# Kernel optimization log

Hardware: AMD Instinct MI355X
Metric: run time of the kernel (lower is better)

The kernel has to match this reference:

```python
import jax, jax.numpy as jnp
import numpy as np

EPS = 1e-3  # Keras BatchNormalization default epsilon


def _conv2d_same(x, w):
    # x: [N,H,W,Cin], w: [kh,kw,Cin,Cout]
    return jax.lax.conv_general_dilated(
        x, w, window_strides=(1, 1), padding='SAME',
        dimension_numbers=('NHWC', 'HWIO', 'NHWC'))


def _hard_sigmoid(x):
    return jnp.clip(0.2 * x + 0.5, 0.0, 1.0)


def _convlstm2d(x, Wx, Wh, b):
    # x: [B,T,H,W,Cin]; Wx: [3,3,Cin,4F]; Wh: [3,3,F,4F]; b: [4F]
    B, T, H, W, Cin = x.shape
    F = Wh.shape[2]
    # precompute input-to-gate convs for all timesteps at once
    xg = _conv2d_same(x.reshape(B * T, H, W, Cin), Wx).reshape(B, T, H, W, 4 * F) + b

    def step(carry, xt):
        h, c = carry
        g = xt + _conv2d_same(h, Wh)
        gi, gf, gc, go = jnp.split(g, 4, axis=-1)  # Keras gate order i,f,c,o
        i = _hard_sigmoid(gi)
        f = _hard_sigmoid(gf)
        o = _hard_sigmoid(go)
        c = f * c + i * jnp.tanh(gc)
        h = o * jnp.tanh(c)
        return (h, c), h

    h0 = jnp.zeros((B, H, W, F), x.dtype)
    (_, _), hs = jax.lax.scan(step, (h0, h0), jnp.moveaxis(xg, 1, 0))
    return jnp.moveaxis(hs, 0, 1)  # [B,T,H,W,F]


def _batchnorm(x, g, be, m, v):
    # inference-mode BN over channel axis
    return (x - m) * (g * jax.lax.rsqrt(v + EPS)) + be


def setup_inputs() -> dict:
    key = jax.random.key(0)
    ks = jax.random.split(key, 10)
    B, T, H, W, C, F, NC = 16, 64, 16, 16, 6, 96, 10
    s = 0.05
    x = jax.random.normal(ks[0], (B, T, H, W, C), jnp.float32)
    Wx0 = jax.random.normal(ks[1], (3, 3, C, 4 * F), jnp.float32) * s
    Wh0 = jax.random.normal(ks[2], (3, 3, F, 4 * F), jnp.float32) * s
    b0 = jnp.zeros((4 * F,), jnp.float32)
    g0 = jnp.ones((F,), jnp.float32)
    be0 = jnp.zeros((F,), jnp.float32)
    m0 = jax.random.normal(ks[3], (F,), jnp.float32) * 0.1
    v0 = jax.random.uniform(ks[4], (F,), jnp.float32) + 0.5
    Wx1 = jax.random.normal(ks[5], (3, 3, F, 4 * F), jnp.float32) * s
    Wh1 = jax.random.normal(ks[6], (3, 3, F, 4 * F), jnp.float32) * s
    b1 = jnp.zeros((4 * F,), jnp.float32)
    g1 = jnp.ones((F,), jnp.float32)
    be1 = jnp.zeros((F,), jnp.float32)
    m1 = jax.random.normal(ks[7], (F,), jnp.float32) * 0.1
    v1 = jax.random.uniform(ks[8], (F,), jnp.float32) + 0.5
    Wd = jax.random.normal(ks[9], (T * H * W * F, NC), jnp.float32) * 0.001
    bd = jnp.zeros((NC,), jnp.float32)
    return dict(x=x, Wx0=Wx0, Wh0=Wh0, b0=b0, g0=g0, be0=be0, m0=m0, v0=v0,
                Wx1=Wx1, Wh1=Wh1, b1=b1, g1=g1, be1=be1, m1=m1, v1=v1,
                Wd=Wd, bd=bd)


def reference(x, Wx0, Wh0, b0, g0, be0, m0, v0,
              Wx1, Wh1, b1, g1, be1, m1, v1, Wd, bd):
    h = _convlstm2d(x, Wx0, Wh0, b0)
    h = _batchnorm(h, g0, be0, m0, v0)
    h = _convlstm2d(h, Wx1, Wh1, b1)
    h = _batchnorm(h, g1, be1, m1, v1)
    B = h.shape[0]
    flat = h.reshape(B, -1)  # Keras Flatten (row-major, channels-last)
    return flat @ Wd + bd
```

## Files before the change

kernel.cpp:

```cpp
#include <hip/hip_runtime.h>
#include <math.h>


typedef __attribute__((ext_vector_type(8))) short     bf16x8;
typedef __attribute__((ext_vector_type(8))) unsigned short u16x8;
typedef __attribute__((ext_vector_type(4))) float     f32x4;
typedef unsigned short u16;

#define RS 393216

__device__ __forceinline__ float hsig(float x) {
    return fminf(fmaxf(0.2f * x + 0.5f, 0.0f), 1.0f);
}
__device__ __forceinline__ float bf2f(u16 u) {
    union { unsigned int i; float f; } v; v.i = ((unsigned int)u) << 16; return v.f;
}
__device__ __forceinline__ u16 f2bf(float f) {
    union { float f; unsigned int i; } v; v.f = f;
    unsigned int r = (v.i + 0x7FFFu + ((v.i >> 16) & 1u)) >> 16;
    return (u16)r;
}

__device__ __forceinline__ void gridbar(unsigned* ctrs, unsigned* epoch,
                                        unsigned k, int blk)
{
    __syncthreads();
    if (threadIdx.x == 0) {
        __builtin_amdgcn_fence(__ATOMIC_RELEASE, "agent");
        __hip_atomic_fetch_add(ctrs + (blk & 63) * 64, 1u,
                               __ATOMIC_RELAXED, __HIP_MEMORY_SCOPE_AGENT);
    }
    if (blk == 0 && threadIdx.x < 64) {
        const unsigned target = k * 256u;
        unsigned sum;
        do {
            unsigned v = __hip_atomic_load(ctrs + threadIdx.x * 64,
                                           __ATOMIC_RELAXED,
                                           __HIP_MEMORY_SCOPE_AGENT);
            sum = v;
#pragma unroll
            for (int m = 1; m < 64; m <<= 1)
                sum += __shfl_xor(sum, m, 64);
            if (sum < target) __builtin_amdgcn_s_sleep(2);
        } while (sum < target);
        if (threadIdx.x == 0)
            __hip_atomic_store(epoch, k, __ATOMIC_RELAXED,
                               __HIP_MEMORY_SCOPE_AGENT);
    }
    if (threadIdx.x == 0) {
        while (__hip_atomic_load(epoch, __ATOMIC_RELAXED,
                                 __HIP_MEMORY_SCOPE_AGENT) < k)
            __builtin_amdgcn_s_sleep(4);
        __builtin_amdgcn_fence(__ATOMIC_ACQUIRE, "agent");
    }
    __syncthreads();
}

__device__ __forceinline__ void xbar(unsigned* slots, int myslot,
                                     unsigned target)
{
    __syncthreads();
    if (threadIdx.x == 0)
        __hip_atomic_fetch_add(slots + myslot * 32, 1u,
                               __ATOMIC_RELAXED, __HIP_MEMORY_SCOPE_AGENT);
    if (threadIdx.x < 32) {
        unsigned sum;
        do {
            unsigned v = __hip_atomic_load(slots + threadIdx.x * 32,
                                           __ATOMIC_RELAXED,
                                           __HIP_MEMORY_SCOPE_AGENT);
            sum = v;
#pragma unroll
            for (int m = 1; m < 32; m <<= 1)
                sum += __shfl_xor(sum, m, 64);
            if (sum < target) __builtin_amdgcn_s_sleep(2);
        } while (sum < target);
        asm volatile("buffer_inv sc0\n\ts_waitcnt vmcnt(0)" ::: "memory");
    }
    __syncthreads();
}

__global__ __launch_bounds__(256) void prep_x(const float* __restrict__ x,
                                              u16* __restrict__ xpad)
{
    const int idx = blockIdx.x * 256 + threadIdx.x;
    const int t = idx >> 12, b = (idx >> 8) & 15, p = idx & 255;
    const float* src = x + (((size_t)b * 64 + t) * 256 + p) * 6;
    u16x8 v = {};
    v[0] = f2bf(src[0]); v[1] = f2bf(src[1]); v[2] = f2bf(src[2]);
    v[3] = f2bf(src[3]); v[4] = f2bf(src[4]); v[5] = f2bf(src[5]);
    *(u16x8*)(xpad + (size_t)idx * 8) = v;
}

__global__ __launch_bounds__(256) void wtransF0(const float* __restrict__ Wx0,
                                                const float* __restrict__ Wh0,
                                                u16* __restrict__ W)
{
    const int idx = blockIdx.x * 256 + threadIdx.x;
    const int e = idx & 7;
    const int lane = (idx >> 3) & 63;
    int r = idx >> 9;
    const int nf = r % 3; r /= 3;
    const int wn = r & 1; r >>= 1;
    const int ks = r % 30;
    const int nt = r / 30;
    const int fr = lane & 15, fg = lane >> 4;
    const int jl = wn * 48 + nf * 16 + fr;
    const int no = (jl / 24) * 96 + nt * 24 + (jl % 24);
    const int k = ks * 32 + fg * 8 + e;
    float v = 0.0f;
    if (k < 96) {
        const int q = k >> 3, c = k & 7;
        if (q < 9 && c < 6) v = Wx0[(q * 6 + c) * 384 + no];
    } else {
        v = Wh0[(k - 96) * 384 + no];
    }
    W[idx] = f2bf(v);
}

__global__ __launch_bounds__(256) void wtransF1(const float* __restrict__ Wx1,
                                                const float* __restrict__ Wh1,
                                                u16* __restrict__ W)
{
    const int idx = blockIdx.x * 256 + threadIdx.x;
    const int e = idx & 7;
    const int lane = (idx >> 3) & 63;
    int r = idx >> 9;
    const int nf = r % 3; r /= 3;
    const int wn = r & 1; r >>= 1;
    const int ks = r % 54;
    const int nt = r / 54;
    const int fr = lane & 15, fg = lane >> 4;
    const int jl = wn * 48 + nf * 16 + fr;
    const int no = (jl / 24) * 96 + nt * 24 + (jl % 24);
    const int k = ks * 32 + fg * 8 + e;
    const float v = (k < 864) ? Wx1[k * 384 + no] : Wh1[(k - 864) * 384 + no];
    W[idx] = f2bf(v);
}

__global__ __launch_bounds__(256) void wtransD(const float* __restrict__ Wd,
                                               u16* __restrict__ WdT)
{
    const int k = blockIdx.x * 256 + threadIdx.x;
    const float* src = Wd + (size_t)k * 10;
#pragma unroll
    for (int nc = 0; nc < 10; ++nc)
        WdT[(size_t)nc * 1572864 + k] = f2bf(src[nc]);
}

__device__ void phase(int t, int m0, int n0, int tidx, char* lds,
    const u16* __restrict__ xpad, u16* __restrict__ h0b,
    u16* __restrict__ h1b, u16* __restrict__ h0bnb, u16* __restrict__ hall,
    const u16* __restrict__ WtF0, const u16* __restrict__ WtF1,
    const float* __restrict__ b0, const float* __restrict__ b1,
    const float* __restrict__ g0, const float* __restrict__ be0,
    const float* __restrict__ mu0, const float* __restrict__ v0,
    const float* __restrict__ g1, const float* __restrict__ be1,
    const float* __restrict__ mu1, const float* __restrict__ v1,
    float (&cregs)[6])
{
    const int half = tidx >> 8;
    const int htid = tidx & 255;
    const bool active = half ? (t < 63) : (t >= 0);

    const u16* in0 = half ? (xpad + (size_t)(t + 1) * 32768)
                          : (h0bnb + (size_t)(t & 1) * RS);
    const u16* in1 = half ? (h0b + (size_t)(t & 1) * RS)
                          : (h1b + (size_t)((t - 1) & 1) * RS);
    u16* hraw_out = half ? (h0b + (size_t)((t + 1) & 1) * RS)
                         : (h1b + (size_t)(t & 1) * RS);
    u16* hbn_out  = half ? (h0bnb + (size_t)((t + 1) & 1) * RS)
                         : (hall + (size_t)(t < 0 ? 0 : t) * RS);

    const int lane = htid & 63;
    const int hw   = htid >> 6;
    const int wm = hw >> 1, wn = hw & 1;
    const int fr = lane & 15, fg = lane >> 4;
    const int arow = htid >> 2, seg = htid & 3;
    const int mg = m0 + arow;
    const int py = (mg >> 4) & 15, px = mg & 15, pb = mg >> 8;
    const int nt = n0 / 96;

    const int   NS0  = half ? 3   : 27;
    const int   MYST = half ? 30  : 54;
    const u16*  Bp   = (half ? WtF0 : WtF1)
                       + (size_t)nt * (MYST * 3072) + wn * 1536 + (lane << 3);

    u16*   AsH  = (u16*)(lds + half * 25600);
    float* accS = (float*)(lds + half * 25600);

    f32x4 acc[2][3];
#pragma unroll
    for (int i = 0; i < 2; ++i)
#pragma unroll
        for (int j = 0; j < 3; ++j) acc[i][j] = (f32x4){0.f, 0.f, 0.f, 0.f};

    auto stageA = [&](int ks, u16x8& va) {
        u16x8 z = {};
        va = z;
        if (half && ks < 3) {
            const int q = ks * 4 + seg;
            const int qd = q / 3;
            const int yy = py + qd - 1;
            const int xx = px + (q - 3 * qd) - 1;
            if (q < 9 && (unsigned)yy < 16u && (unsigned)xx < 16u)
                va = *(const u16x8*)(in0 + (size_t)((pb << 8) + yy * 16 + xx) * 8);
        } else {
            const int s = (ks < NS0) ? ks : ks - NS0;
            const u16* src = (ks < NS0) ? in0 : in1;
            const int q = s / 3;
            const int c0v = (s - 3 * q) * 32 + seg * 8;
            const int qd = q / 3;
            const int yy = py + qd - 1;
            const int xx = px + (q - 3 * qd) - 1;
            if ((unsigned)yy < 16u && (unsigned)xx < 16u)
                va = *(const u16x8*)(src + (size_t)((pb << 8) + yy * 16 + xx) * 96 + c0v);
        }
    };
    auto ldswA = [&](int buf, u16x8& va) {
        *(u16x8*)(AsH + buf * 2560 + arow * 40 + seg * 8) = va;
    };
    auto loadB = [&](int ks, bf16x8 (&bq)[3]) {
#pragma unroll
        for (int nf = 0; nf < 3; ++nf)
            bq[nf] = *(const bf16x8*)(Bp + ks * 3072 + nf * 512);
    };
    auto dofrag = [&](int buf, bf16x8 (&bq)[3]) {
        const u16* A = AsH + buf * 2560;
        bf16x8 af[2];
#pragma unroll
        for (int mf = 0; mf < 2; ++mf)
            af[mf] = *(const bf16x8*)(A + (wm * 32 + mf * 16 + fr) * 40 + fg * 8);

        __builtin_amdgcn_s_setprio(1);
#pragma unroll
        for (int mf = 0; mf < 2; ++mf)
#pragma unroll
            for (int nf = 0; nf < 3; ++nf)
                acc[mf][nf] = __builtin_amdgcn_mfma_f32_16x16x32_bf16(
                    af[mf], bq[nf], acc[mf][nf], 0, 0, 0);
        __builtin_amdgcn_s_setprio(0);
    };

    u16x8 vaA, vaB;
    bf16x8 bqE[3], bqO[3], tE[3], tO[3];

    if (active) {
        stageA(0, vaA); stageA(1, vaB);
        ldswA(0, vaA);  ldswA(1, vaB);
        loadB(0, bqE);  loadB(1, bqO);
    }
    __syncthreads();

    for (int j = 0; j < 27; ++j) {
        const int ks = 2 * j;
        if (active && ks < MYST) {
            const bool more = (ks + 2 < MYST);
            if (more) {
                stageA(ks + 2, vaA);
                stageA(ks + 3, vaB);
                loadB(ks + 2, tE);
                loadB(ks + 3, tO);
            }
            dofrag(ks & 3, bqE);
            dofrag((ks + 1) & 3, bqO);
            if (more) {
                ldswA((ks + 2) & 3, vaA);
                ldswA((ks + 3) & 3, vaB);
#pragma unroll
                for (int nf = 0; nf < 3; ++nf) {
                    bqE[nf] = tE[nf];
                    bqO[nf] = tO[nf];
                }
            }
        }
        __syncthreads();
    }

    if (active) {
        const float* bias = half ? b0 : b1;
#pragma unroll
        for (int nf = 0; nf < 3; ++nf) {
            const int col = wn * 48 + nf * 16 + fr;
            const float bi = bias[(col / 24) * 96 + nt * 24 + (col % 24)];
#pragma unroll
            for (int mf = 0; mf < 2; ++mf) {
                const int row = wm * 32 + mf * 16 + fg * 4;
#pragma unroll
                for (int r = 0; r < 4; ++r)
                    accS[(row + r) * 100 + col] = acc[mf][nf][r] + bi;
            }
        }
    }
    __syncthreads();

    if (active) {
        const float* gam = half ? g0 : g1;
        const float* bet = half ? be0 : be1;
        const float* muv = half ? mu0 : mu1;
        const float* var = half ? v0  : v1;
#pragma unroll
        for (int q = 0; q < 6; ++q) {
            const int item = htid + 256 * q;
            const int r = item / 24, fl = item - r * 24;
            const float gi = accS[r * 100 + fl];
            const float gf = accS[r * 100 + 24 + fl];
            const float gc = accS[r * 100 + 48 + fl];
            const float go = accS[r * 100 + 72 + fl];
            const int f = nt * 24 + fl;
            const float i_ = hsig(gi);
            const float f_ = hsig(gf);
            const float o_ = hsig(go);
            const float c_ = f_ * cregs[q] + i_ * tanhf(gc);
            const float h_ = o_ * tanhf(c_);
            cregs[q] = c_;
            hraw_out[(size_t)(m0 + r) * 96 + f] = f2bf(h_);
            const float s = gam[f] * rsqrtf(var[f] + 1e-3f);
            hbn_out[(size_t)(m0 + r) * 96 + f] =
                f2bf((h_ - muv[f]) * s + bet[f]);
        }
    }
}

__global__ __launch_bounds__(512, 1) void fused(
    unsigned* bctrs, unsigned* bepoch, unsigned* reg8, unsigned* xslots,
    const u16* xpad, u16* h0b, u16* h1b, u16* h0bnb, u16* hall,
    const u16* WtF0, const u16* WtF1,
    const float* b0, const float* b1,
    const float* g0, const float* be0, const float* mu0, const float* v0,
    const float* g1, const float* be1, const float* mu1, const float* v1)
{
    __shared__ char lds[51200];
    __shared__ unsigned shinfo[3];
    const int blk = blockIdx.x;

    if (threadIdx.x == 0) {
        unsigned xcc;
        asm volatile("s_getreg_b32 %0, hwreg(HW_REG_XCC_ID)" : "=s"(xcc));
        xcc &= 7u;
        unsigned slot = __hip_atomic_fetch_add(reg8 + xcc * 64, 1u,
                                               __ATOMIC_RELAXED,
                                               __HIP_MEMORY_SCOPE_AGENT);
        shinfo[0] = xcc; shinfo[1] = slot;
    }
    gridbar(bctrs, bepoch, 1, blk);
    if (threadIdx.x == 0) {
        unsigned ok = 1;
#pragma unroll
        for (int k = 0; k < 8; ++k)
            ok &= (__hip_atomic_load(reg8 + k * 64, __ATOMIC_RELAXED,
                                     __HIP_MEMORY_SCOPE_AGENT) == 32u);
        shinfo[2] = ok;
    }
    __syncthreads();
    const unsigned grp  = shinfo[0];
    const unsigned slot = shinfo[1];
    const bool grouped  = (shinfo[2] != 0u);

    float cregs[6] = {0.f, 0.f, 0.f, 0.f, 0.f, 0.f};

    if (grouped) {
        const int m0 = (int)grp * 512 + (int)(slot >> 2) * 64;
        const int n0 = (int)(slot & 3) * 96;
        unsigned* gs = xslots + grp * 1024;
        unsigned bar = 0;
        for (int t = -1; t < 64; ++t) {
            phase(t, m0, n0, threadIdx.x, lds, xpad, h0b, h1b, h0bnb, hall,
                  WtF0, WtF1, b0, b1, g0, be0, mu0, v0, g1, be1, mu1, v1,
                  cregs);
            xbar(gs, (int)slot, (++bar) * 32u);
        }
    } else {
        const int m0 = (blk >> 2) * 64;
        const int n0 = (blk & 3) * 96;
        unsigned bar = 1;
        for (int t = -1; t < 64; ++t) {
            phase(t, m0, n0, threadIdx.x, lds, xpad, h0b, h1b, h0bnb, hall,
                  WtF0, WtF1, b0, b1, g0, be0, mu0, v0, g1, be1, mu1, v1,
                  cregs);
            gridbar(bctrs, bepoch, ++bar, blk);
        }
    }
}

__global__ __launch_bounds__(512, 1) void stepF(int t,
    const u16* xpad, u16* h0b, u16* h1b, u16* h0bnb, u16* hall,
    const u16* WtF0, const u16* WtF1,
    const float* b0, const float* b1,
    const float* g0, const float* be0, const float* mu0, const float* v0,
    const float* g1, const float* be1, const float* mu1, const float* v1,
    float* c0g, float* c1g)
{
    __shared__ char lds[51200];
    const int m0 = (blockIdx.x >> 2) * 64;
    const int n0 = (blockIdx.x & 3) * 96;
    const int half = threadIdx.x >> 8;
    const int htid = threadIdx.x & 255;
    const int nt = n0 / 96;
    float* cst = half ? c0g : c1g;

    float cregs[6];
#pragma unroll
    for (int q = 0; q < 6; ++q) {
        const int item = htid + 256 * q;
        const int r = item / 24, fl = item - r * 24;
        cregs[q] = cst[(size_t)(m0 + r) * 96 + nt * 24 + fl];
    }
    phase(t, m0, n0, threadIdx.x, lds, xpad, h0b, h1b, h0bnb, hall,
          WtF0, WtF1, b0, b1, g0, be0, mu0, v0, g1, be1, mu1, v1, cregs);
#pragma unroll
    for (int q = 0; q < 6; ++q) {
        const int item = htid + 256 * q;
        const int r = item / 24, fl = item - r * 24;
        cst[(size_t)(m0 + r) * 96 + nt * 24 + fl] = cregs[q];
    }
}

__global__ void dense_partial(const u16* __restrict__ hall,
                              const u16* __restrict__ WdT,
                              float* __restrict__ partial)
{
    const int k0 = blockIdx.x * 2048;
    const int tt = k0 / 24576;
    const int r0 = k0 - tt * 24576;
    const int th = threadIdx.x;
    const int b  = th / 10;
    const int nc = th - b * 10;
    const u16* hp = hall + (size_t)(tt * 16 + b) * 24576 + r0;
    const u16* wp = WdT + (size_t)nc * 1572864 + k0;
    float acc = 0.0f;
    for (int j = 0; j < 2048; j += 8) {
        const u16x8 hv = *(const u16x8*)(hp + j);
        const u16x8 wv = *(const u16x8*)(wp + j);
#pragma unroll
        for (int u = 0; u < 8; ++u)
            acc = fmaf(bf2f(hv[u]), bf2f(wv[u]), acc);
    }
    partial[blockIdx.x * 160 + th] = acc;
}

__global__ void dense_reduce(const float* __restrict__ partial,
                             const float* __restrict__ bd,
                             float* __restrict__ out)
{
    const int t = threadIdx.x;
    const int nc = t - (t / 10) * 10;
    float acc = bd[nc];
    for (int p = 0; p < 768; ++p) acc += partial[p * 160 + t];
    out[t] = acc;
}

extern "C" void kernel_launch(void* const* d_in, const int* in_sizes, int n_in,
                              void* d_out, int out_size, void* d_ws, size_t ws_size,
                              hipStream_t stream)
{
    const float* x    = (const float*)d_in[0];
    const float* Wx0  = (const float*)d_in[1];
    const float* Wh0  = (const float*)d_in[2];
    const float* b0p  = (const float*)d_in[3];
    const float* g0p  = (const float*)d_in[4];
    const float* be0p = (const float*)d_in[5];
    const float* mu0p = (const float*)d_in[6];
    const float* v0p  = (const float*)d_in[7];
    const float* Wx1  = (const float*)d_in[8];
    const float* Wh1  = (const float*)d_in[9];
    const float* b1p  = (const float*)d_in[10];
    const float* g1p  = (const float*)d_in[11];
    const float* be1p = (const float*)d_in[12];
    const float* mu1p = (const float*)d_in[13];
    const float* v1p  = (const float*)d_in[14];
    const float* Wd   = (const float*)d_in[15];
    const float* bd   = (const float*)d_in[16];
    float* out = (float*)d_out;

    char* base = (char*)d_ws;
    u16*   h0b    = (u16*)(base);
    u16*   h1b    = (u16*)(base + 1572864);
    u16*   h0bnb  = (u16*)(base + 3145728);
    float* c0g    = (float*)(base + 4718592);
    float* c1g    = (float*)(base + 6291456);
    u16*   xpad   = (u16*)(base + 7864320);
    u16*   WtF0   = (u16*)(base + 12058624);
    u16*   WtF1   = (u16*)(base + 12795904);
    u16*   hall   = (u16*)(base + 14123008);
    float* part   = (float*)(base + 64454656);
    u16*   WdT    = (u16*)(base + 64946176);
    unsigned* bctrs  = (unsigned*)(base + 96403456);
    unsigned* bepoch = (unsigned*)(base + 96419840);
    unsigned* reg8   = (unsigned*)(base + 96420096);
    unsigned* xslots = (unsigned*)(base + 96422144);

    hipMemsetAsync(base, 0, 7864320, stream);
    hipMemsetAsync(bctrs, 0, 51456, stream);

    prep_x  <<<1024, 256, 0, stream>>>(x, xpad);
    wtransF0<<<1440, 256, 0, stream>>>(Wx0, Wh0, WtF0);
    wtransF1<<<2592, 256, 0, stream>>>(Wx1, Wh1, WtF1);
    wtransD <<<6144, 256, 0, stream>>>(Wd, WdT);

    void* args[] = {
        (void*)&bctrs, (void*)&bepoch, (void*)&reg8, (void*)&xslots,
        (void*)&xpad, (void*)&h0b, (void*)&h1b, (void*)&h0bnb, (void*)&hall,
        (void*)&WtF0, (void*)&WtF1, (void*)&b0p, (void*)&b1p,
        (void*)&g0p, (void*)&be0p, (void*)&mu0p, (void*)&v0p,
        (void*)&g1p, (void*)&be1p, (void*)&mu1p, (void*)&v1p
    };
    hipError_t ce = hipLaunchCooperativeKernel((void*)fused, dim3(256),
                                               dim3(512), args, 0, stream);
    if (ce != hipSuccess) {
        (void)hipGetLastError();
        for (int t = -1; t < 64; ++t) {
            stepF<<<256, 512, 0, stream>>>(t, xpad, h0b, h1b, h0bnb, hall,
                                           WtF0, WtF1, b0p, b1p,
                                           g0p, be0p, mu0p, v0p,
                                           g1p, be1p, mu1p, v1p, c0g, c1g);
        }
    }

    dense_partial<<<768, 160, 0, stream>>>(hall, WdT, part);
    dense_reduce <<<1, 160, 0, stream>>>(part, bd, out);
}
```

Baseline: 1.743 ms.

## Rebalance K-steps between block halves by splitting layer-1 GEMM across both halves

Previously one half of the block did the 54-step layer-1 gate GEMM while the other did the 30-step layer-0 GEMM, so the shorter half idled for the last 24 steps. Now each half runs 42 steps: half 0 does layer-1 steps 0-41, and half 1 does layer-1 steps 42-53 plus all of layer 0. The two layer-1 partial sums are combined through LDS before the LSTM epilogue. This adds an extra accumulator set, more register pressure, one more barrier and an LDS reduction pass.

```diff
diff --git a/kernel.cpp b/kernel.cpp
--- a/kernel.cpp
+++ b/kernel.cpp
@@ -161,16 +161,11 @@
 {
     const int half = tidx >> 8;
     const int htid = tidx & 255;
-    const bool active = half ? (t < 63) : (t >= 0);
-
-    const u16* in0 = half ? (xpad + (size_t)(t + 1) * 32768)
-                          : (h0bnb + (size_t)(t & 1) * RS);
-    const u16* in1 = half ? (h0b + (size_t)(t & 1) * RS)
-                          : (h1b + (size_t)((t - 1) & 1) * RS);
-    u16* hraw_out = half ? (h0b + (size_t)((t + 1) & 1) * RS)
-                         : (h1b + (size_t)(t & 1) * RS);
-    u16* hbn_out  = half ? (h0bnb + (size_t)((t + 1) & 1) * RS)
-                         : (hall + (size_t)(t < 0 ? 0 : t) * RS);
+
+    const u16* xin = xpad + (size_t)(t + 1 < 64 ? t + 1 : 63) * 32768;
+    const u16* c0B = h0b   + (size_t)(t & 1) * RS;
+    const u16* c1A = h0bnb + (size_t)(t & 1) * RS;
+    const u16* c1B = h1b   + (size_t)((t - 1) & 1) * RS;
 
     const int lane = htid & 63;
     const int hw   = htid >> 6;
@@ -181,51 +176,73 @@
     const int py = (mg >> 4) & 15, px = mg & 15, pb = mg >> 8;
     const int nt = n0 / 96;
 
-    const int   NS0  = half ? 3   : 27;
-    const int   MYST = half ? 30  : 54;
-    const u16*  Bp   = (half ? WtF0 : WtF1)
-                       + (size_t)nt * (MYST * 3072) + wn * 1536 + (lane << 3);
-
-    u16*   AsH  = (u16*)(lds + half * 25600);
-    float* accS = (float*)(lds + half * 25600);
-
-    f32x4 acc[2][3];
+    const u16* Bp1 = WtF1 + (size_t)nt * (54 * 3072) + wn * 1536 + (lane << 3);
+    const u16* Bp0 = WtF0 + (size_t)nt * (30 * 3072) + wn * 1536 + (lane << 3);
+
+    u16*   AsH   = (u16*)(lds + half * 25600);
+    float* accS0 = (float*)lds;
+    float* accS1 = (float*)(lds + 25600);
+
+    f32x4 acc1[2][3], acc0[2][3];
 #pragma unroll
     for (int i = 0; i < 2; ++i)
 #pragma unroll
-        for (int j = 0; j < 3; ++j) acc[i][j] = (f32x4){0.f, 0.f, 0.f, 0.f};
-
-    auto stageA = [&](int ks, u16x8& va) {
+        for (int j = 0; j < 3; ++j) {
+            acc1[i][j] = (f32x4){0.f, 0.f, 0.f, 0.f};
+            acc0[i][j] = (f32x4){0.f, 0.f, 0.f, 0.f};
+        }
+
+    auto mapw = [&](int w, int& conv, int& ks) {
+        if (half == 0)      { conv = 1; ks = w; }
+        else if (w < 12)    { conv = 1; ks = 42 + w; }
+        else                { conv = 0; ks = w - 12; }
+    };
+    auto stageA = [&](int conv, int ks, u16x8& va) {
         u16x8 z = {};
         va = z;
-        if (half && ks < 3) {
-            const int q = ks * 4 + seg;
-            const int qd = q / 3;
-            const int yy = py + qd - 1;
-            const int xx = px + (q - 3 * qd) - 1;
-            if (q < 9 && (unsigned)yy < 16u && (unsigned)xx < 16u)
-                va = *(const u16x8*)(in0 + (size_t)((pb << 8) + yy * 16 + xx) * 8);
+        if (conv == 0) {
+            if (ks < 3) {
+                const int q = ks * 4 + seg;
+                const int qd = q / 3;
+                const int yy = py + qd - 1;
+                const int xx = px + (q - 3 * qd) - 1;
+                if (q < 9 && (unsigned)yy < 16u && (unsigned)xx < 16u)
+                    va = *(const u16x8*)(xin +
+                        (size_t)((pb << 8) + yy * 16 + xx) * 8);
+            } else {
+                const int s = ks - 3;
+                const int q = s / 3;
+                const int c0v = (s - 3 * q) * 32 + seg * 8;
+                const int qd = q / 3;
+                const int yy = py + qd - 1;
+                const int xx = px + (q - 3 * qd) - 1;
+                if ((unsigned)yy < 16u && (unsigned)xx < 16u)
+                    va = *(const u16x8*)(c0B +
+                        (size_t)((pb << 8) + yy * 16 + xx) * 96 + c0v);
+            }
         } else {
-            const int s = (ks < NS0) ? ks : ks - NS0;
-            const u16* src = (ks < NS0) ? in0 : in1;
+            const int s = (ks < 27) ? ks : ks - 27;
+            const u16* src = (ks < 27) ? c1A : c1B;
             const int q = s / 3;
             const int c0v = (s - 3 * q) * 32 + seg * 8;
             const int qd = q / 3;
             const int yy = py + qd - 1;
             const int xx = px + (q - 3 * qd) - 1;
             if ((unsigned)yy < 16u && (unsigned)xx < 16u)
-                va = *(const u16x8*)(src + (size_t)((pb << 8) + yy * 16 + xx) * 96 + c0v);
+                va = *(const u16x8*)(src +
+                    (size_t)((pb << 8) + yy * 16 + xx) * 96 + c0v);
         }
     };
     auto ldswA = [&](int buf, u16x8& va) {
         *(u16x8*)(AsH + buf * 2560 + arow * 40 + seg * 8) = va;
     };
-    auto loadB = [&](int ks, bf16x8 (&bq)[3]) {
+    auto loadB = [&](int conv, int ks, bf16x8 (&bq)[3]) {
+        const u16* Bp = conv ? Bp1 : Bp0;
 #pragma unroll
         for (int nf = 0; nf < 3; ++nf)
             bq[nf] = *(const bf16x8*)(Bp + ks * 3072 + nf * 512);
     };
-    auto dofrag = [&](int buf, bf16x8 (&bq)[3]) {
+    auto dofrag = [&](int buf, bf16x8 (&bq)[3], f32x4 (&acc)[2][3]) {
         const u16* A = AsH + buf * 2560;
         bf16x8 af[2];
 #pragma unroll
@@ -243,70 +260,51 @@
     };
 
     u16x8 vaA, vaB;
-    bf16x8 bqE[3], bqO[3], tE[3], tO[3];
-
-    if (active) {
-        stageA(0, vaA); stageA(1, vaB);
-        ldswA(0, vaA);  ldswA(1, vaB);
-        loadB(0, bqE);  loadB(1, bqO);
-    }
-    __syncthreads();
-
-    for (int j = 0; j < 27; ++j) {
-        const int ks = 2 * j;
-        if (active && ks < MYST) {
-            const bool more = (ks + 2 < MYST);
-            if (more) {
-                stageA(ks + 2, vaA);
-                stageA(ks + 3, vaB);
-                loadB(ks + 2, tE);
-                loadB(ks + 3, tO);
-            }
-            dofrag(ks & 3, bqE);
-            dofrag((ks + 1) & 3, bqO);
-            if (more) {
-                ldswA((ks + 2) & 3, vaA);
-                ldswA((ks + 3) & 3, vaB);
-#pragma unroll
-                for (int nf = 0; nf < 3; ++nf) {
-                    bqE[nf] = tE[nf];
-                    bqO[nf] = tO[nf];
-                }
-            }
-        }
+    bf16x8 bqE[3], bqO[3];
+
+    {
+        int cv, ck;
+        mapw(0, cv, ck); stageA(cv, ck, vaA); loadB(cv, ck, bqE);
+        mapw(1, cv, ck); stageA(cv, ck, vaB); loadB(cv, ck, bqO);
+        ldswA(0, vaA); ldswA(1, vaB);
+    }
+    __syncthreads();
+
+    for (int j = 0; j < 21; ++j) {
+        const int w = 2 * j;
+        const bool more = (w + 2 < 42);
+        int cvA = 0, ckA = 0, cvB = 0, ckB = 0;
+        if (more) {
+            mapw(w + 2, cvA, ckA); stageA(cvA, ckA, vaA);
+            mapw(w + 3, cvB, ckB); stageA(cvB, ckB, vaB);
+        }
+        {
+            int c, k; mapw(w, c, k);
+            if (c) dofrag(w & 3, bqE, acc1);
+            else   dofrag(w & 3, bqE, acc0);
+            if (more) loadB(cvA, ckA, bqE);
+        }
+        {
+            int c, k; mapw(w + 1, c, k);
+            if (c) dofrag((w + 1) & 3, bqO, acc1);
+            else   dofrag((w + 1) & 3, bqO, acc0);
+            if (more) loadB(cvB, ckB, bqO);
+        }
+        if (more) { ldswA((w + 2) & 3, vaA); ldswA((w + 3) & 3, vaB); }
         __syncthreads();
     }
 
-    if (active) {
-        const float* bias = half ? b0 : b1;
-#pragma unroll
-        for (int nf = 0; nf < 3; ++nf) {
-            const int col = wn * 48 + nf * 16 + fr;
-            const float bi = bias[(col / 24) * 96 + nt * 24 + (col % 24)];
-#pragma unroll
-            for (int mf = 0; mf < 2; ++mf) {
-                const int row = wm * 32 + mf * 16 + fg * 4;
-#pragma unroll
-                for (int r = 0; r < 4; ++r)
-                    accS[(row + r) * 100 + col] = acc[mf][nf][r] + bi;
-            }
-        }
-    }
-    __syncthreads();
-
-    if (active) {
-        const float* gam = half ? g0 : g1;
-        const float* bet = half ? be0 : be1;
-        const float* muv = half ? mu0 : mu1;
-        const float* var = half ? v0  : v1;
+    auto E2 = [&](float* aS, const float* gam, const float* bet,
+                  const float* muv, const float* var,
+                  u16* hraw, u16* hbn) {
 #pragma unroll
         for (int q = 0; q < 6; ++q) {
             const int item = htid + 256 * q;
             const int r = item / 24, fl = item - r * 24;
-            const float gi = accS[r * 100 + fl];
-            const float gf = accS[r * 100 + 24 + fl];
-            const float gc = accS[r * 100 + 48 + fl];
-            const float go = accS[r * 100 + 72 + fl];
+            const float gi = aS[r * 100 + fl];
+            const float gf = aS[r * 100 + 24 + fl];
+            const float gc = aS[r * 100 + 48 + fl];
+            const float go = aS[r * 100 + 72 + fl];
             const int f = nt * 24 + fl;
             const float i_ = hsig(gi);
             const float f_ = hsig(gf);
@@ -314,11 +312,69 @@
             const float c_ = f_ * cregs[q] + i_ * tanhf(gc);
             const float h_ = o_ * tanhf(c_);
             cregs[q] = c_;
-            hraw_out[(size_t)(m0 + r) * 96 + f] = f2bf(h_);
+            hraw[(size_t)(m0 + r) * 96 + f] = f2bf(h_);
             const float s = gam[f] * rsqrtf(var[f] + 1e-3f);
-            hbn_out[(size_t)(m0 + r) * 96 + f] =
+            hbn[(size_t)(m0 + r) * 96 + f] =
                 f2bf((h_ - muv[f]) * s + bet[f]);
         }
+    };
+
+    if (half == 1) {
+        if (t >= 0) {
+#pragma unroll
+            for (int nf = 0; nf < 3; ++nf) {
+                const int col = wn * 48 + nf * 16 + fr;
+#pragma unroll
+                for (int mf = 0; mf < 2; ++mf) {
+                    const int row = wm * 32 + mf * 16 + fg * 4;
+#pragma unroll
+                    for (int r = 0; r < 4; ++r)
+                        accS0[(row + r) * 100 + col] = acc1[mf][nf][r];
+                }
+            }
+        }
+        if (t < 63) {
+#pragma unroll
+            for (int nf = 0; nf < 3; ++nf) {
+                const int col = wn * 48 + nf * 16 + fr;
+                const float bi = b0[(col / 24) * 96 + nt * 24 + (col % 24)];
+#pragma unroll
+                for (int mf = 0; mf < 2; ++mf) {
+                    const int row = wm * 32 + mf * 16 + fg * 4;
+#pragma unroll
+                    for (int r = 0; r < 4; ++r)
+                        accS1[(row + r) * 100 + col] = acc0[mf][nf][r] + bi;
+                }
+            }
+        }
+    }
+    __syncthreads();
+
+    if (half == 0 && t >= 0) {
+#pragma unroll
+        for (int nf = 0; nf < 3; ++nf) {
+            const int col = wn * 48 + nf * 16 + fr;
+            const float bi = b1[(col / 24) * 96 + nt * 24 + (col % 24)];
+#pragma unroll
+            for (int mf = 0; mf < 2; ++mf) {
+                const int row = wm * 32 + mf * 16 + fg * 4;
+#pragma unroll
+                for (int r = 0; r < 4; ++r)
+                    accS0[(row + r) * 100 + col] += acc1[mf][nf][r] + bi;
+            }
+        }
+    }
+    if (half == 1 && t < 63) {
+        E2(accS1, g0, be0, mu0, v0,
+           h0b + (size_t)((t + 1) & 1) * RS,
+           h0bnb + (size_t)((t + 1) & 1) * RS);
+    }
+    __syncthreads();
+
+    if (half == 0 && t >= 0) {
+        E2(accS0, g1, be1, mu1, v1,
+           h1b + (size_t)(t & 1) * RS,
+           hall + (size_t)(t < 0 ? 0 : t) * RS);
     }
 }
 
```

Measured after the change: 2.433 ms. 1.4x slower.
